# Performance work log

Measured on AMD Instinct MI355X. Metric: run time of the kernel, lower is better.

## Reference

```python
import jax, jax.numpy as jnp
import numpy as np

D_MODEL = 1024
NUM_HEADS = 16
D_HEAD = D_MODEL // NUM_HEADS
SCALE = D_HEAD ** -0.5
B, S = 2, 2048


def setup_inputs() -> dict:
    key = jax.random.key(0)
    ks = jax.random.split(key, 9)
    # Xavier-uniform-like scale for square weights: sqrt(6/(fan_in+fan_out))
    lim = float(np.sqrt(6.0 / (D_MODEL + D_MODEL)))
    def w(k):
        return jax.random.uniform(k, (D_MODEL, D_MODEL), jnp.float32, -lim, lim)
    def b(k):
        return jax.random.normal(k, (D_MODEL,), jnp.float32) * 0.02
    return {
        "query": jax.random.normal(ks[0], (B, S, D_MODEL), jnp.float32),
        "Wq": w(ks[1]), "bq": b(ks[2]),
        "Wk": w(ks[3]), "bk": b(ks[4]),
        "Wv": w(ks[5]), "bv": b(ks[6]),
        "Wo": w(ks[7]), "bo": b(ks[8]),
    }


def reference(query, Wq, bq, Wk, bk, Wv, bv, Wo, bo):
    Bsz, Sl, _ = query.shape
    # torch Linear: y = x @ W.T + b
    q = query @ Wq.T + bq
    k = query @ Wk.T + bk
    v = query @ Wv.T + bv
    # split heads -> [B, H, S, Dh]
    def split(t):
        return t.reshape(Bsz, Sl, NUM_HEADS, D_HEAD).transpose(0, 2, 1, 3)
    q, k, v = split(q), split(k), split(v)
    # regular attention path: full [B,H,S,S] score matrix, no causal mask
    attn_weights = jnp.einsum("bhqd,bhkd->bhqk", q, k) * SCALE
    attn_probs = jax.nn.softmax(attn_weights, axis=-1)
    attn_output = jnp.einsum("bhqk,bhkd->bhqd", attn_probs, v)
    # merge heads
    merged = attn_output.transpose(0, 2, 1, 3).reshape(Bsz, Sl, D_MODEL)
    return merged @ Wo.T + bo
```

## Files before the change

### kernel.cpp

```cpp
#include <hip/hip_runtime.h>
#include <cstdint>
#include <cstddef>

typedef __bf16 bf16;
typedef __bf16 bf16x8 __attribute__((ext_vector_type(8)));
typedef float f32x4 __attribute__((ext_vector_type(4)));

#define DMODEL 1024
#define HEADS  16
#define DH     64
#define BATCH  2
#define SEQ    2048
#define MTOT   (BATCH*SEQ)
#define LDQKV  3072

#define QKSCALE  0.18033688f
#define M2SHIFT  11.541560f

typedef __attribute__((address_space(1))) void gas_void;
typedef __attribute__((address_space(3))) void las_void;
#define GLOAD_LDS(gsrc, ldst) \
  __builtin_amdgcn_global_load_lds((gas_void*)(gsrc), (las_void*)(ldst), 16, 0, 0)

__device__ __forceinline__ f32x4 mfma16(bf16x8 a, bf16x8 b, f32x4 c) {
  return __builtin_amdgcn_mfma_f32_16x16x32_bf16(a, b, c, 0, 0, 0);
}

__device__ __forceinline__ float exp2_fast(float x) {
  float r;
  asm("v_exp_f32 %0, %1" : "=v"(r) : "v"(x));
  return r;
}

__device__ __forceinline__ bf16x8 cvt8(float4 a, float4 b) {
  bf16x8 v;
  v[0] = (bf16)a.x; v[1] = (bf16)a.y; v[2] = (bf16)a.z; v[3] = (bf16)a.w;
  v[4] = (bf16)b.x; v[5] = (bf16)b.y; v[6] = (bf16)b.z; v[7] = (bf16)b.w;
  return v;
}

__global__ __launch_bounds__(256) void k_prep(
    const float* __restrict__ x, const float* __restrict__ Wq, const float* __restrict__ Wk,
    const float* __restrict__ Wv, const float* __restrict__ bq, const float* __restrict__ bk,
    const float* __restrict__ bv, const float* __restrict__ Wo,
    bf16* __restrict__ xbf, bf16* __restrict__ Wqkv, float* __restrict__ bqkv,
    bf16* __restrict__ wo) {
  const int blk = blockIdx.x, tid = threadIdx.x;
  if (blk < 2048) {
    const int i = blk * 256 + tid;
    const float4* p = (const float4*)x;
    ((bf16x8*)xbf)[i] = cvt8(p[2*i], p[2*i+1]);
  } else if (blk < 3584) {
    const int i = (blk - 2048) * 256 + tid;
    const int row = i >> 7;
    const int c   = (i & 127) * 8;
    const float* src;
    if (row < 1024)       src = Wq + (size_t)row * 1024 + c;
    else if (row < 2048)  src = Wk + (size_t)(row - 1024) * 1024 + c;
    else                  src = Wv + (size_t)(row - 2048) * 1024 + c;
    float4 a = ((const float4*)src)[0], b = ((const float4*)src)[1];
    ((bf16x8*)Wqkv)[i] = cvt8(a, b);
    if (i < 3072) {
      float bb;
      if (i < 1024)      bb = bq[i];
      else if (i < 2048) bb = bk[i - 1024];
      else               bb = bv[i - 2048];
      bqkv[i] = bb;
    }
  } else {
    const int i = (blk - 3584) * 256 + tid;
    const float4* p = (const float4*)Wo;
    ((bf16x8*)wo)[i] = cvt8(p[2*i], p[2*i+1]);
  }
}

template <int QSCALE, int OUTF32>
__global__ __launch_bounds__(256) void k_gemm_bt(const bf16* __restrict__ A,
                                                 const bf16* __restrict__ B,
                                                 const float* __restrict__ bias,
                                                 void* __restrict__ Cout,
                                                 int N, int K) {
  __shared__ bf16 Alds[128 * 32];
  __shared__ bf16 Blds[128 * 32];
  const int tid  = threadIdx.x;
  const int lane = tid & 63;
  const int w    = tid >> 6;
  const int wr   = w >> 1, wc = w & 1;
  const int l15  = lane & 15, lg = lane >> 4;
  const int bm = blockIdx.x, bn = blockIdx.y;

  f32x4 acc[4][4];
#pragma unroll
  for (int i = 0; i < 4; ++i)
#pragma unroll
    for (int j = 0; j < 4; ++j) acc[i][j] = (f32x4){0.f, 0.f, 0.f, 0.f};

  const int r = tid >> 2;
  const int c = (tid & 3) * 8;
  const bf16* aptr0 = A + ((size_t)bm * 128 + r) * K + c;
  const bf16* aptr1 = A + ((size_t)bm * 128 + 64 + r) * K + c;
  const bf16* bptr0 = B + ((size_t)bn * 128 + r) * K + c;
  const bf16* bptr1 = B + ((size_t)bn * 128 + 64 + r) * K + c;

  for (int kt = 0; kt < K / 32; ++kt) {
    __syncthreads();
    GLOAD_LDS(aptr0, Alds + tid * 8);
    GLOAD_LDS(aptr1, Alds + 2048 + tid * 8);
    GLOAD_LDS(bptr0, Blds + tid * 8);
    GLOAD_LDS(bptr1, Blds + 2048 + tid * 8);
    aptr0 += 32; aptr1 += 32; bptr0 += 32; bptr1 += 32;
    __syncthreads();

    bf16x8 af[4], bfr[4];
#pragma unroll
    for (int i = 0; i < 4; ++i)
      af[i] = *(const bf16x8*)(Alds + (wr * 64 + i * 16 + l15) * 32 + lg * 8);
#pragma unroll
    for (int j = 0; j < 4; ++j)
      bfr[j] = *(const bf16x8*)(Blds + (wc * 64 + j * 16 + l15) * 32 + lg * 8);
#pragma unroll
    for (int i = 0; i < 4; ++i)
#pragma unroll
      for (int j = 0; j < 4; ++j)
        acc[i][j] = mfma16(af[i], bfr[j], acc[i][j]);
  }

#pragma unroll
  for (int j = 0; j < 4; ++j) {
    const int col = bn * 128 + wc * 64 + j * 16 + l15;
    const float bv = bias[col];
    const float scale = (QSCALE && col < 1024) ? QKSCALE : 1.0f;
#pragma unroll
    for (int i = 0; i < 4; ++i) {
      const int row0 = bm * 128 + wr * 64 + i * 16 + lg * 4;
#pragma unroll
      for (int rr = 0; rr < 4; ++rr) {
        const float v = (acc[i][j][rr] + bv) * scale;
        const size_t off = (size_t)(row0 + rr) * N + col;
        if (OUTF32) ((float*)Cout)[off] = v;
        else        ((bf16*)Cout)[off]  = (bf16)v;
      }
    }
  }
}

__global__ __launch_bounds__(256) void k_transpose_v(const bf16* __restrict__ qkv,
                                                     bf16* __restrict__ vt) {
  __shared__ bf16 tile[64][72];
  const int bh = blockIdx.x, st = blockIdx.y;
  const int b = bh >> 4, h = bh & 15;
  const int tid = threadIdx.x;
  const int r = tid >> 2, c0 = (tid & 3) * 16;
  const bf16* src = qkv + (size_t)(b * SEQ + st * 64 + r) * LDQKV + 2048 + h * DH + c0;
  *(bf16x8*)&tile[r][c0]     = ((const bf16x8*)src)[0];
  *(bf16x8*)&tile[r][c0 + 8] = ((const bf16x8*)src)[1];
  __syncthreads();
  const int d = tid >> 2, s0 = (tid & 3) * 16;
  bf16x8 o0, o1;
#pragma unroll
  for (int j = 0; j < 8; ++j) o0[j] = tile[s0 + j][d];
#pragma unroll
  for (int j = 0; j < 8; ++j) o1[j] = tile[s0 + 8 + j][d];
  bf16* dst = vt + ((size_t)bh * DH + d) * SEQ + st * 64 + s0;
  *(bf16x8*)dst       = o0;
  *(bf16x8*)(dst + 8) = o1;
}

__global__ __launch_bounds__(256) void k_attn(const bf16* __restrict__ qkv,
                                              const bf16* __restrict__ vt,
                                              bf16* __restrict__ attnout) {
  __shared__ bf16 Klds[2][64 * 64];
  __shared__ bf16 Vtlds[2][64 * 64];
  __shared__ bf16 Plds[4][16 * 64];

  const int orig = blockIdx.x;
  const int wgid = (orig & 7) * 128 + (orig >> 3);
  const int bh = wgid >> 5;
  const int qt = wgid & 31;
  const int b = bh >> 4, h = bh & 15;
  const int tid = threadIdx.x;
  const int lane = tid & 63, w = tid >> 6;
  const int l15 = lane & 15, lg = lane >> 4;
  const int r7 = l15 & 7;
  const int qbase = qt * 64 + w * 16;

  const int sr = tid >> 3;
  const int ss = tid & 7;

  auto STAGE = [&](int buf, int t) {
    const int kb = t * 64;
#pragma unroll
    for (int u = 0; u < 2; ++u) {
      const int row = u * 32 + sr;
      const int slot = ss ^ (row & 7);
      const bf16* ksrc = qkv + (size_t)(b * SEQ + kb + row) * LDQKV + 1024 + h * DH + slot * 8;
      GLOAD_LDS(ksrc, Klds[buf] + u * 2048 + tid * 8);
      const bf16* vsrc = vt + ((size_t)bh * DH + row) * SEQ + kb + slot * 8;
      GLOAD_LDS(vsrc, Vtlds[buf] + u * 2048 + tid * 8);
    }
  };

  bf16x8 qf[2];
#pragma unroll
  for (int kc = 0; kc < 2; ++kc)
    qf[kc] = *(const bf16x8*)(qkv + (size_t)(b * SEQ + qbase + l15) * LDQKV
                              + h * DH + kc * 32 + lg * 8);

  f32x4 oacc[4];
#pragma unroll
  for (int dt = 0; dt < 4; ++dt) oacc[dt] = (f32x4){0.f, 0.f, 0.f, 0.f};
  float l_r[4];
#pragma unroll
  for (int rr = 0; rr < 4; ++rr) l_r[rr] = 0.f;

  STAGE(0, 0);
  __syncthreads();

  int cur = 0;
  for (int t = 0; t < SEQ / 64; ++t) {
    if (t + 1 < SEQ / 64) STAGE(cur ^ 1, t + 1);

    const bf16* Kb = Klds[cur];
    const bf16* Vb = Vtlds[cur];

    f32x4 sacc[4];
    __builtin_amdgcn_s_setprio(1);
#pragma unroll
    for (int kt = 0; kt < 4; ++kt) {
      const bf16* krow = Kb + (kt * 16 + l15) * 64;
      bf16x8 kf0 = *(const bf16x8*)(krow + ((lg ^ r7) * 8));
      bf16x8 kf1 = *(const bf16x8*)(krow + (((4 + lg) ^ r7) * 8));
      f32x4 z = (f32x4){0.f, 0.f, 0.f, 0.f};
      z = mfma16(qf[0], kf0, z);
      z = mfma16(qf[1], kf1, z);
      sacc[kt] = z;
    }
    __builtin_amdgcn_s_setprio(0);

    float p[4][4];
#pragma unroll
    for (int rr = 0; rr < 4; ++rr)
#pragma unroll
      for (int kt = 0; kt < 4; ++kt) {
        const float e = exp2_fast(sacc[kt][rr] - M2SHIFT);
        p[kt][rr] = e;
        l_r[rr] += e;
      }

    char* pb = (char*)Plds[w];
#pragma unroll
    for (int kt = 0; kt < 4; ++kt)
#pragma unroll
      for (int rr = 0; rr < 4; ++rr) {
        const int q = lg * 4 + rr;
        const int k = kt * 16 + l15;
        const int off = (q * 128 + k * 2) ^ ((q & 7) << 4);
        *(bf16*)(pb + off) = (bf16)p[kt][rr];
      }

    const bf16* prow = (const bf16*)Plds[w] + l15 * 64;
    bf16x8 pa0 = *(const bf16x8*)(prow + ((lg ^ r7) * 8));
    bf16x8 pa1 = *(const bf16x8*)(prow + (((4 + lg) ^ r7) * 8));
    __builtin_amdgcn_s_setprio(1);
#pragma unroll
    for (int dt = 0; dt < 4; ++dt) {
      const bf16* vrow = Vb + (dt * 16 + l15) * 64;
      bf16x8 vf0 = *(const bf16x8*)(vrow + ((lg ^ r7) * 8));
      bf16x8 vf1 = *(const bf16x8*)(vrow + (((4 + lg) ^ r7) * 8));
      oacc[dt] = mfma16(pa0, vf0, oacc[dt]);
      oacc[dt] = mfma16(pa1, vf1, oacc[dt]);
    }
    __builtin_amdgcn_s_setprio(0);

    __syncthreads();
    cur ^= 1;
  }

#pragma unroll
  for (int rr = 0; rr < 4; ++rr) {
    float rs = l_r[rr];
    rs += __shfl_xor(rs, 1);
    rs += __shfl_xor(rs, 2);
    rs += __shfl_xor(rs, 4);
    rs += __shfl_xor(rs, 8);
    const float inv = 1.0f / rs;
    const int row = qbase + lg * 4 + rr;
#pragma unroll
    for (int dt = 0; dt < 4; ++dt)
      attnout[(size_t)(b * SEQ + row) * DMODEL + h * DH + dt * 16 + l15] =
          (bf16)(oacc[dt][rr] * inv);
  }
}

extern "C" void kernel_launch(void* const* d_in, const int* in_sizes, int n_in,
                              void* d_out, int out_size, void* d_ws, size_t ws_size,
                              hipStream_t stream) {
  (void)in_sizes; (void)n_in; (void)out_size; (void)ws_size;
  const float* query = (const float*)d_in[0];
  const float* Wq = (const float*)d_in[1];
  const float* bq = (const float*)d_in[2];
  const float* Wk = (const float*)d_in[3];
  const float* bk = (const float*)d_in[4];
  const float* Wv = (const float*)d_in[5];
  const float* bv = (const float*)d_in[6];
  const float* Wo = (const float*)d_in[7];
  const float* bo = (const float*)d_in[8];

  char* ws = (char*)d_ws;
  bf16*  xbf  = (bf16*)(ws);
  bf16*  attn = (bf16*)(ws);
  bf16*  wqkv = (bf16*)(ws + 8388608);
  bf16*  wo   = (bf16*)(ws + 14680064);
  float* bqkv = (float*)(ws + 16777216);
  bf16*  qkv  = (bf16*)(ws + 16842752);
  bf16*  vt   = (bf16*)(ws + 42008576);

  k_prep<<<4096, 256, 0, stream>>>(query, Wq, Wk, Wv, bq, bk, bv, Wo,
                                   xbf, wqkv, bqkv, wo);
  k_gemm_bt<1, 0><<<dim3(32, 24), 256, 0, stream>>>(xbf, wqkv, bqkv, (void*)qkv, 3072, 1024);
  k_transpose_v<<<dim3(32, 32), 256, 0, stream>>>(qkv, vt);
  k_attn<<<1024, 256, 0, stream>>>(qkv, vt, attn);
  k_gemm_bt<0, 1><<<dim3(32, 8), 256, 0, stream>>>(attn, wo, bo, d_out, 1024, 1024);
}
```

Baseline: 216.6 us.

## Deepen GEMM K-tile to 64 with XOR-swizzled LDS and smaller output-projection tiles

The bf16 GEMM kernel now stages 64-wide K slices per iteration instead of 32, which halves the number of barrier pairs. It applies an XOR swizzle on LDS column slots to avoid bank conflicts on the fragment reads. The tile height is now a template parameter, and the output projection uses 64-row tiles so it launches twice as many blocks and fills more CUs. The cost is more LDS per block, and the smaller tiles give less reuse per block in the output GEMM.

After: 213.2 us. About the same (-1.6%).

```diff
diff --git a/kernel.cpp b/kernel.cpp
--- a/kernel.cpp
+++ b/kernel.cpp
@@ -74,14 +74,14 @@
   }
 }
 
-template <int QSCALE, int OUTF32>
+template <int BM, int QSCALE, int OUTF32>
 __global__ __launch_bounds__(256) void k_gemm_bt(const bf16* __restrict__ A,
                                                  const bf16* __restrict__ B,
                                                  const float* __restrict__ bias,
                                                  void* __restrict__ Cout,
                                                  int N, int K) {
-  __shared__ bf16 Alds[128 * 32];
-  __shared__ bf16 Blds[128 * 32];
+  __shared__ bf16 Alds[BM * 64];
+  __shared__ bf16 Blds[128 * 64];
   const int tid  = threadIdx.x;
   const int lane = tid & 63;
   const int w    = tid >> 6;
@@ -89,40 +89,60 @@
   const int l15  = lane & 15, lg = lane >> 4;
   const int bm = blockIdx.x, bn = blockIdx.y;
 
-  f32x4 acc[4][4];
-#pragma unroll
-  for (int i = 0; i < 4; ++i)
+  f32x4 acc[BM / 32][4];
+#pragma unroll
+  for (int i = 0; i < BM / 32; ++i)
 #pragma unroll
     for (int j = 0; j < 4; ++j) acc[i][j] = (f32x4){0.f, 0.f, 0.f, 0.f};
 
-  const int r = tid >> 2;
-  const int c = (tid & 3) * 8;
-  const bf16* aptr0 = A + ((size_t)bm * 128 + r) * K + c;
-  const bf16* aptr1 = A + ((size_t)bm * 128 + 64 + r) * K + c;
-  const bf16* bptr0 = B + ((size_t)bn * 128 + r) * K + c;
-  const bf16* bptr1 = B + ((size_t)bn * 128 + 64 + r) * K + c;
-
-  for (int kt = 0; kt < K / 32; ++kt) {
+  const int srow = tid >> 3;
+  const int sslot = tid & 7;
+  const bf16* aptr[BM / 32];
+  const bf16* bptr[4];
+#pragma unroll
+  for (int u = 0; u < BM / 32; ++u) {
+    const int row = u * 32 + srow;
+    aptr[u] = A + (size_t)(bm * BM + row) * K + ((sslot ^ (row & 7)) * 8);
+  }
+#pragma unroll
+  for (int u = 0; u < 4; ++u) {
+    const int row = u * 32 + srow;
+    bptr[u] = B + (size_t)(bn * 128 + row) * K + ((sslot ^ (row & 7)) * 8);
+  }
+
+  for (int kt = 0; kt < K / 64; ++kt) {
     __syncthreads();
-    GLOAD_LDS(aptr0, Alds + tid * 8);
-    GLOAD_LDS(aptr1, Alds + 2048 + tid * 8);
-    GLOAD_LDS(bptr0, Blds + tid * 8);
-    GLOAD_LDS(bptr1, Blds + 2048 + tid * 8);
-    aptr0 += 32; aptr1 += 32; bptr0 += 32; bptr1 += 32;
+#pragma unroll
+    for (int u = 0; u < BM / 32; ++u) {
+      GLOAD_LDS(aptr[u], Alds + u * 2048 + tid * 8);
+      aptr[u] += 64;
+    }
+#pragma unroll
+    for (int u = 0; u < 4; ++u) {
+      GLOAD_LDS(bptr[u], Blds + u * 2048 + tid * 8);
+      bptr[u] += 64;
+    }
     __syncthreads();
 
-    bf16x8 af[4], bfr[4];
-#pragma unroll
-    for (int i = 0; i < 4; ++i)
-      af[i] = *(const bf16x8*)(Alds + (wr * 64 + i * 16 + l15) * 32 + lg * 8);
-#pragma unroll
-    for (int j = 0; j < 4; ++j)
-      bfr[j] = *(const bf16x8*)(Blds + (wc * 64 + j * 16 + l15) * 32 + lg * 8);
-#pragma unroll
-    for (int i = 0; i < 4; ++i)
-#pragma unroll
-      for (int j = 0; j < 4; ++j)
-        acc[i][j] = mfma16(af[i], bfr[j], acc[i][j]);
+#pragma unroll
+    for (int kk = 0; kk < 2; ++kk) {
+      bf16x8 af[BM / 32], bfr[4];
+#pragma unroll
+      for (int i = 0; i < BM / 32; ++i) {
+        const int r = wr * (BM / 2) + i * 16 + l15;
+        af[i] = *(const bf16x8*)(Alds + r * 64 + (((kk * 4 + lg) ^ (r & 7)) * 8));
+      }
+#pragma unroll
+      for (int j = 0; j < 4; ++j) {
+        const int r = wc * 64 + j * 16 + l15;
+        bfr[j] = *(const bf16x8*)(Blds + r * 64 + (((kk * 4 + lg) ^ (r & 7)) * 8));
+      }
+#pragma unroll
+      for (int i = 0; i < BM / 32; ++i)
+#pragma unroll
+        for (int j = 0; j < 4; ++j)
+          acc[i][j] = mfma16(af[i], bfr[j], acc[i][j]);
+    }
   }
 
 #pragma unroll
@@ -131,8 +151,8 @@
     const float bv = bias[col];
     const float scale = (QSCALE && col < 1024) ? QKSCALE : 1.0f;
 #pragma unroll
-    for (int i = 0; i < 4; ++i) {
-      const int row0 = bm * 128 + wr * 64 + i * 16 + lg * 4;
+    for (int i = 0; i < BM / 32; ++i) {
+      const int row0 = bm * BM + wr * (BM / 2) + i * 16 + lg * 4;
 #pragma unroll
       for (int rr = 0; rr < 4; ++rr) {
         const float v = (acc[i][j][rr] + bv) * scale;
@@ -317,8 +337,8 @@
 
   k_prep<<<4096, 256, 0, stream>>>(query, Wq, Wk, Wv, bq, bk, bv, Wo,
                                    xbf, wqkv, bqkv, wo);
-  k_gemm_bt<1, 0><<<dim3(32, 24), 256, 0, stream>>>(xbf, wqkv, bqkv, (void*)qkv, 3072, 1024);
+  k_gemm_bt<128, 1, 0><<<dim3(32, 24), 256, 0, stream>>>(xbf, wqkv, bqkv, (void*)qkv, 3072, 1024);
   k_transpose_v<<<dim3(32, 32), 256, 0, stream>>>(qkv, vt);
   k_attn<<<1024, 256, 0, stream>>>(qkv, vt, attn);
-  k_gemm_bt<0, 1><<<dim3(32, 8), 256, 0, stream>>>(attn, wo, bo, d_out, 1024, 1024);
-}
+  k_gemm_bt<64, 0, 1><<<dim3(64, 8), 256, 0, stream>>>(attn, wo, bo, d_out, 1024, 1024);
+}
```
